# Optimization experiments

Measured on AMD Instinct MI355X. Metric: run time of the kernel, lower is better.

The kernel has to match this reference:

```python
import jax, jax.numpy as jnp
import numpy as np


def setup_inputs() -> dict:
    key = jax.random.key(0)
    ks = jax.random.split(key, 6)
    B, d, S = 256, 512, 196  # batch, hidden dim, spatial locations (14x14)
    return {
        "memory_state": jax.random.normal(ks[0], (B, d), dtype=jnp.float32),
        "ctrl_state": jax.random.normal(ks[1], (B, d), dtype=jnp.float32),
        "kb_proj": jax.random.normal(ks[2], (B, d, S), dtype=jnp.float32),
        "W_concat": jax.random.normal(ks[3], (d, d), dtype=jnp.float32) * (1.0 / np.sqrt(d)),
        "b_concat": jax.random.normal(ks[4], (d,), dtype=jnp.float32) * 0.01,
        "w_attn": jax.random.normal(ks[5], (d,), dtype=jnp.float32) * (1.0 / np.sqrt(d)),
    }


def reference(memory_state, ctrl_state, kb_proj, W_concat, b_concat, w_attn):
    # I_elements: [B, S, d] -- elementwise gating of knowledge base by memory
    I_t = memory_state[:, :, None] * kb_proj           # [B, d, S]
    I_t = jnp.transpose(I_t, (0, 2, 1))                # [B, S, d]
    # concat_layer (torch Linear: x @ W^T + b) + residual with kb_proj
    concat = jnp.einsum('bsd,ed->bse', I_t, W_concat) + b_concat
    concat = concat + jnp.transpose(kb_proj, (0, 2, 1))  # [B, S, d]
    # attention logits: (concat * ctrl) @ w_attn -> [B, S]
    rai = jnp.einsum('bsd,d->bs', concat * ctrl_state[:, None, :], w_attn)
    rvi = jax.nn.softmax(rai, axis=1)                  # [B, S]
    # attention-weighted sum over spatial locations -> [B, d]
    read_vector = jnp.einsum('bs,bds->bd', rvi, kb_proj)
    return read_vector
```

## Files before the change

kernel.cpp:

```cpp
#include <hip/hip_runtime.h>
#include <math.h>

#define B 256
#define D 512
#define S 196
#define NCH 8
#define TC 16
#define NT 13

__global__ __launch_bounds__(256) void k_gemm2(
    const float* __restrict__ ctrl, const float* __restrict__ w_attn,
    const float* __restrict__ W, float* __restrict__ gpart) {
    __shared__ float u_s[64][8];
    const int ce = blockIdx.x >> 6;
    const int dh = (blockIdx.x >> 5) & 1;
    const int b0 = (blockIdx.x & 31) * 8;
    const int t = threadIdx.x;
    const int d = dh * 256 + t;
#pragma unroll
    for (int k = t; k < 512; k += 256) {
        const int j = k & 7, el = k >> 3;
        const int e = ce * 64 + el;
        u_s[el][j] = ctrl[(size_t)(b0 + j) * D + e] * w_attn[e];
    }
    __syncthreads();
    float a[8];
#pragma unroll
    for (int j = 0; j < 8; ++j) a[j] = 0.f;
    for (int e0 = 0; e0 < 64; e0 += 4) {
        float wv[4];
#pragma unroll
        for (int i = 0; i < 4; ++i)
            wv[i] = W[(size_t)(ce * 64 + e0 + i) * D + d];
#pragma unroll
        for (int i = 0; i < 4; ++i) {
            const float4 ua = *(const float4*)&u_s[e0 + i][0];
            const float4 ub = *(const float4*)&u_s[e0 + i][4];
            a[0] += ua.x * wv[i]; a[1] += ua.y * wv[i];
            a[2] += ua.z * wv[i]; a[3] += ua.w * wv[i];
            a[4] += ub.x * wv[i]; a[5] += ub.y * wv[i];
            a[6] += ub.z * wv[i]; a[7] += ub.w * wv[i];
        }
    }
#pragma unroll
    for (int j = 0; j < 8; ++j)
        gpart[((size_t)(b0 + j) * NCH + ce) * D + d] = a[j];
}

__global__ __launch_bounds__(1024, 1) void k_online(
    const float* __restrict__ kb, const float* __restrict__ gpart,
    const float* __restrict__ mem, const float* __restrict__ ctrl,
    const float* __restrict__ w_attn, float* __restrict__ out) {
    __shared__ float tile[2][D][TC + 1];
    __shared__ float pr[TC][65];
    __shared__ float rai_t[TC];
    __shared__ float p_s[D];
    __shared__ float oa[2][D];
    __shared__ float Zs[2];
    const int b = blockIdx.x;
    const int t = threadIdx.x;
    const float* base = kb + (size_t)b * D * S;

    const int ld_d = t >> 2, ld_jq = t & 3;
    const int col_lo = 4 * ld_jq;

    float4 v0 = *(const float4*)(base + (size_t)ld_d * S + col_lo);
    float4 v1 = *(const float4*)(base + (size_t)(ld_d + 256) * S + col_lo);

    if (t < D) {
        float s = 0.f;
#pragma unroll
        for (int ce = 0; ce < NCH; ++ce)
            s += gpart[((size_t)b * NCH + ce) * D + t];
        p_s[t] = mem[(size_t)b * D + t] * s +
                 ctrl[(size_t)b * D + t] * w_attn[t];
    }

    tile[0][ld_d][col_lo + 0] = v0.x; tile[0][ld_d][col_lo + 1] = v0.y;
    tile[0][ld_d][col_lo + 2] = v0.z; tile[0][ld_d][col_lo + 3] = v0.w;
    tile[0][ld_d + 256][col_lo + 0] = v1.x;
    tile[0][ld_d + 256][col_lo + 1] = v1.y;
    tile[0][ld_d + 256][col_lo + 2] = v1.z;
    tile[0][ld_d + 256][col_lo + 3] = v1.w;
    __syncthreads();

    const int col = t & 15, dseg = t >> 4;
    const int wvx = t >> 6, l = t & 63;
    const int dow = t >> 1, sh = t & 1;

    float mrun = -1e30f, Zrun = 0.f, oacc = 0.f;

    for (int j = 0; j < NT; ++j) {
        const int cur = j & 1;
        float4 u0 = {0.f, 0.f, 0.f, 0.f}, u1 = {0.f, 0.f, 0.f, 0.f};
        if (j + 1 < NT) {
            const int c0 = (j + 1) * TC + col_lo;
            if (c0 + 3 < S) {
                u0 = *(const float4*)(base + (size_t)ld_d * S + c0);
                u1 = *(const float4*)(base + (size_t)(ld_d + 256) * S + c0);
            }
        }
        float a = 0.f;
#pragma unroll
        for (int i = 0; i < 8; ++i)
            a += p_s[dseg * 8 + i] * tile[cur][dseg * 8 + i][col];
        pr[col][dseg] = a;
        __syncthreads();
        {
            float vs = pr[wvx][l];
#pragma unroll
            for (int o = 1; o < 64; o <<= 1) vs += __shfl_xor(vs, o, 64);
            if (l == 0)
                rai_t[wvx] = (j * TC + wvx < S) ? vs : -1e30f;
        }
        __syncthreads();
        float mt = rai_t[0];
#pragma unroll
        for (int i = 1; i < TC; ++i) mt = fmaxf(mt, rai_t[i]);
        const float mnew = fmaxf(mrun, mt);
        const float f = __expf(mrun - mnew);
        float wexp[8];
        float zadd = 0.f;
#pragma unroll
        for (int i = 0; i < 8; ++i) {
            wexp[i] = __expf(rai_t[sh * 8 + i] - mnew);
            zadd += wexp[i];
        }
        Zrun = Zrun * f + zadd;
        oacc *= f;
#pragma unroll
        for (int i = 0; i < 8; ++i)
            oacc += wexp[i] * tile[cur][dow][sh * 8 + i];
        mrun = mnew;
        if (j + 1 < NT) {
            const int nb = cur ^ 1;
            tile[nb][ld_d][col_lo + 0] = u0.x;
            tile[nb][ld_d][col_lo + 1] = u0.y;
            tile[nb][ld_d][col_lo + 2] = u0.z;
            tile[nb][ld_d][col_lo + 3] = u0.w;
            tile[nb][ld_d + 256][col_lo + 0] = u1.x;
            tile[nb][ld_d + 256][col_lo + 1] = u1.y;
            tile[nb][ld_d + 256][col_lo + 2] = u1.z;
            tile[nb][ld_d + 256][col_lo + 3] = u1.w;
        }
        __syncthreads();
    }

    oa[sh][dow] = oacc;
    if (t == 0) Zs[0] = Zrun;
    if (t == 1) Zs[1] = Zrun;
    __syncthreads();
    if (t < D)
        out[(size_t)b * D + t] = (oa[0][t] + oa[1][t]) / (Zs[0] + Zs[1]);
}

extern "C" void kernel_launch(void* const* d_in, const int* in_sizes, int n_in,
                              void* d_out, int out_size, void* d_ws, size_t ws_size,
                              hipStream_t stream) {
    const float* mem  = (const float*)d_in[0];
    const float* ctrl = (const float*)d_in[1];
    const float* kb   = (const float*)d_in[2];
    const float* W    = (const float*)d_in[3];
    const float* wat  = (const float*)d_in[5];
    float* out = (float*)d_out;

    float* gpart = (float*)d_ws;

    k_gemm2 <<<512, 256,  0, stream>>>(ctrl, wat, W, gpart);
    k_online<<<B,   1024, 0, stream>>>(kb, gpart, mem, ctrl, wat, out);
}
```

Measured before the change: 178.5 us.

## Keep kb tiles in registers and reduce logits with wave shuffles

The online-softmax kernel no longer stages kb tiles in shared memory. Each thread keeps its two float4 slices in registers, computes partial logits, reduces them with cross-lane shuffles plus one small shared buffer, and accumulates the weighted sum directly from registers. That removes the shared tile traffic and one barrier per tile. The pre-GEMM is also re-tiled into 2048 blocks with 16 e-chunks and float4 W loads, which drops its shared memory and barrier but doubles the partial sums that k_online must read and add.

```diff
diff --git a/kernel.cpp b/kernel.cpp
--- a/kernel.cpp
+++ b/kernel.cpp
@@ -4,68 +4,59 @@
 #define B 256
 #define D 512
 #define S 196
-#define NCH 8
+#define NCH 16
 #define TC 16
 #define NT 13
 
-__global__ __launch_bounds__(256) void k_gemm2(
+__global__ __launch_bounds__(256) void k_gemm(
     const float* __restrict__ ctrl, const float* __restrict__ w_attn,
     const float* __restrict__ W, float* __restrict__ gpart) {
-    __shared__ float u_s[64][8];
-    const int ce = blockIdx.x >> 6;
-    const int dh = (blockIdx.x >> 5) & 1;
-    const int b0 = (blockIdx.x & 31) * 8;
+    const int bid = blockIdx.x;
+    const int ce = bid & 15;
+    const int dq4 = (bid >> 4) & 3;
+    const int b0 = (bid >> 6) * 8;
     const int t = threadIdx.x;
-    const int d = dh * 256 + t;
+    const int j = t >> 5, dqi = t & 31;
+    const int d = dq4 * 128 + dqi * 4;
+    const int e0 = ce * 32;
+    float u[32];
 #pragma unroll
-    for (int k = t; k < 512; k += 256) {
-        const int j = k & 7, el = k >> 3;
-        const int e = ce * 64 + el;
-        u_s[el][j] = ctrl[(size_t)(b0 + j) * D + e] * w_attn[e];
+    for (int k = 0; k < 8; ++k) {
+        const float4 cv =
+            *(const float4*)(ctrl + (size_t)(b0 + j) * D + e0 + 4 * k);
+        const float4 wv = *(const float4*)(w_attn + e0 + 4 * k);
+        u[4 * k + 0] = cv.x * wv.x; u[4 * k + 1] = cv.y * wv.y;
+        u[4 * k + 2] = cv.z * wv.z; u[4 * k + 3] = cv.w * wv.w;
     }
-    __syncthreads();
-    float a[8];
+    float4 a = {0.f, 0.f, 0.f, 0.f};
 #pragma unroll
-    for (int j = 0; j < 8; ++j) a[j] = 0.f;
-    for (int e0 = 0; e0 < 64; e0 += 4) {
-        float wv[4];
-#pragma unroll
-        for (int i = 0; i < 4; ++i)
-            wv[i] = W[(size_t)(ce * 64 + e0 + i) * D + d];
-#pragma unroll
-        for (int i = 0; i < 4; ++i) {
-            const float4 ua = *(const float4*)&u_s[e0 + i][0];
-            const float4 ub = *(const float4*)&u_s[e0 + i][4];
-            a[0] += ua.x * wv[i]; a[1] += ua.y * wv[i];
-            a[2] += ua.z * wv[i]; a[3] += ua.w * wv[i];
-            a[4] += ub.x * wv[i]; a[5] += ub.y * wv[i];
-            a[6] += ub.z * wv[i]; a[7] += ub.w * wv[i];
-        }
+    for (int e = 0; e < 32; ++e) {
+        const float4 w4 = *(const float4*)(W + (size_t)(e0 + e) * D + d);
+        a.x += u[e] * w4.x; a.y += u[e] * w4.y;
+        a.z += u[e] * w4.z; a.w += u[e] * w4.w;
     }
-#pragma unroll
-    for (int j = 0; j < 8; ++j)
-        gpart[((size_t)(b0 + j) * NCH + ce) * D + d] = a[j];
+    *(float4*)&gpart[((size_t)(b0 + j) * NCH + ce) * D + d] = a;
 }
 
 __global__ __launch_bounds__(1024, 1) void k_online(
     const float* __restrict__ kb, const float* __restrict__ gpart,
     const float* __restrict__ mem, const float* __restrict__ ctrl,
     const float* __restrict__ w_attn, float* __restrict__ out) {
-    __shared__ float tile[2][D][TC + 1];
-    __shared__ float pr[TC][65];
-    __shared__ float rai_t[TC];
     __shared__ float p_s[D];
-    __shared__ float oa[2][D];
-    __shared__ float Zs[2];
+    __shared__ float wpr[2][16][20];
     const int b = blockIdx.x;
     const int t = threadIdx.x;
+    const int l = t & 63, wv = t >> 6;
+    const int rl = t >> 2;
+    const int jq = t & 3;
     const float* base = kb + (size_t)b * D * S;
 
-    const int ld_d = t >> 2, ld_jq = t & 3;
-    const int col_lo = 4 * ld_jq;
-
-    float4 v0 = *(const float4*)(base + (size_t)ld_d * S + col_lo);
-    float4 v1 = *(const float4*)(base + (size_t)(ld_d + 256) * S + col_lo);
+    float4 ca, cb, na, nb;
+    {
+        const int c0 = 4 * jq;
+        ca = *(const float4*)(base + (size_t)rl * S + c0);
+        cb = *(const float4*)(base + (size_t)(rl + 256) * S + c0);
+    }
 
     if (t < D) {
         float s = 0.f;
@@ -75,83 +66,78 @@
         p_s[t] = mem[(size_t)b * D + t] * s +
                  ctrl[(size_t)b * D + t] * w_attn[t];
     }
+    __syncthreads();
+    const float p0 = p_s[rl], p1 = p_s[rl + 256];
 
-    tile[0][ld_d][col_lo + 0] = v0.x; tile[0][ld_d][col_lo + 1] = v0.y;
-    tile[0][ld_d][col_lo + 2] = v0.z; tile[0][ld_d][col_lo + 3] = v0.w;
-    tile[0][ld_d + 256][col_lo + 0] = v1.x;
-    tile[0][ld_d + 256][col_lo + 1] = v1.y;
-    tile[0][ld_d + 256][col_lo + 2] = v1.z;
-    tile[0][ld_d + 256][col_lo + 3] = v1.w;
-    __syncthreads();
+    float mrun = -1e30f, Zrun = 0.f, o0 = 0.f, o1 = 0.f;
 
-    const int col = t & 15, dseg = t >> 4;
-    const int wvx = t >> 6, l = t & 63;
-    const int dow = t >> 1, sh = t & 1;
-
-    float mrun = -1e30f, Zrun = 0.f, oacc = 0.f;
-
-    for (int j = 0; j < NT; ++j) {
-        const int cur = j & 1;
-        float4 u0 = {0.f, 0.f, 0.f, 0.f}, u1 = {0.f, 0.f, 0.f, 0.f};
-        if (j + 1 < NT) {
-            const int c0 = (j + 1) * TC + col_lo;
+    for (int jt = 0; jt < NT; ++jt) {
+        const int buf = jt & 1;
+        if (jt + 1 < NT) {
+            const int c0 = (jt + 1) * TC + 4 * jq;
             if (c0 + 3 < S) {
-                u0 = *(const float4*)(base + (size_t)ld_d * S + c0);
-                u1 = *(const float4*)(base + (size_t)(ld_d + 256) * S + c0);
+                na = *(const float4*)(base + (size_t)rl * S + c0);
+                nb = *(const float4*)(base + (size_t)(rl + 256) * S + c0);
+            } else {
+                na = make_float4(0.f, 0.f, 0.f, 0.f);
+                nb = make_float4(0.f, 0.f, 0.f, 0.f);
             }
         }
-        float a = 0.f;
+        float lp[4];
+        lp[0] = p0 * ca.x + p1 * cb.x;
+        lp[1] = p0 * ca.y + p1 * cb.y;
+        lp[2] = p0 * ca.z + p1 * cb.z;
+        lp[3] = p0 * ca.w + p1 * cb.w;
 #pragma unroll
-        for (int i = 0; i < 8; ++i)
-            a += p_s[dseg * 8 + i] * tile[cur][dseg * 8 + i][col];
-        pr[col][dseg] = a;
-        __syncthreads();
-        {
-            float vs = pr[wvx][l];
-#pragma unroll
-            for (int o = 1; o < 64; o <<= 1) vs += __shfl_xor(vs, o, 64);
-            if (l == 0)
-                rai_t[wvx] = (j * TC + wvx < S) ? vs : -1e30f;
+        for (int o = 4; o < 64; o <<= 1) {
+            lp[0] += __shfl_xor(lp[0], o, 64);
+            lp[1] += __shfl_xor(lp[1], o, 64);
+            lp[2] += __shfl_xor(lp[2], o, 64);
+            lp[3] += __shfl_xor(lp[3], o, 64);
+        }
+        if (l < 4) {
+            wpr[buf][4 * l + 0][wv] = lp[0];
+            wpr[buf][4 * l + 1][wv] = lp[1];
+            wpr[buf][4 * l + 2][wv] = lp[2];
+            wpr[buf][4 * l + 3][wv] = lp[3];
         }
         __syncthreads();
-        float mt = rai_t[0];
+        const float4 q0 = *(const float4*)&wpr[buf][l & 15][0];
+        const float4 q1 = *(const float4*)&wpr[buf][l & 15][4];
+        const float4 q2 = *(const float4*)&wpr[buf][l & 15][8];
+        const float4 q3 = *(const float4*)&wpr[buf][l & 15][12];
+        float r = ((q0.x + q0.y) + (q0.z + q0.w)) +
+                  ((q1.x + q1.y) + (q1.z + q1.w)) +
+                  ((q2.x + q2.y) + (q2.z + q2.w)) +
+                  ((q3.x + q3.y) + (q3.z + q3.w));
+        r = (jt * TC + (l & 15) < S) ? r : -1e30f;
+        float mt = r;
 #pragma unroll
-        for (int i = 1; i < TC; ++i) mt = fmaxf(mt, rai_t[i]);
+        for (int o = 1; o < 16; o <<= 1)
+            mt = fmaxf(mt, __shfl_xor(mt, o, 64));
         const float mnew = fmaxf(mrun, mt);
         const float f = __expf(mrun - mnew);
-        float wexp[8];
-        float zadd = 0.f;
-#pragma unroll
-        for (int i = 0; i < 8; ++i) {
-            wexp[i] = __expf(rai_t[sh * 8 + i] - mnew);
-            zadd += wexp[i];
-        }
-        Zrun = Zrun * f + zadd;
-        oacc *= f;
-#pragma unroll
-        for (int i = 0; i < 8; ++i)
-            oacc += wexp[i] * tile[cur][dow][sh * 8 + i];
         mrun = mnew;
-        if (j + 1 < NT) {
-            const int nb = cur ^ 1;
-            tile[nb][ld_d][col_lo + 0] = u0.x;
-            tile[nb][ld_d][col_lo + 1] = u0.y;
-            tile[nb][ld_d][col_lo + 2] = u0.z;
-            tile[nb][ld_d][col_lo + 3] = u0.w;
-            tile[nb][ld_d + 256][col_lo + 0] = u1.x;
-            tile[nb][ld_d + 256][col_lo + 1] = u1.y;
-            tile[nb][ld_d + 256][col_lo + 2] = u1.z;
-            tile[nb][ld_d + 256][col_lo + 3] = u1.w;
-        }
-        __syncthreads();
+        const int sb = l & 48;
+        const float r0 = __shfl(r, sb + 4 * jq + 0, 64);
+        const float r1 = __shfl(r, sb + 4 * jq + 1, 64);
+        const float r2 = __shfl(r, sb + 4 * jq + 2, 64);
+        const float r3 = __shfl(r, sb + 4 * jq + 3, 64);
+        const float w0 = __expf(r0 - mnew), w1 = __expf(r1 - mnew);
+        const float w2 = __expf(r2 - mnew), w3 = __expf(r3 - mnew);
+        Zrun = Zrun * f + ((w0 + w1) + (w2 + w3));
+        o0 = o0 * f + (w0 * ca.x + w1 * ca.y + w2 * ca.z + w3 * ca.w);
+        o1 = o1 * f + (w0 * cb.x + w1 * cb.y + w2 * cb.z + w3 * cb.w);
+        ca = na; cb = nb;
     }
 
-    oa[sh][dow] = oacc;
-    if (t == 0) Zs[0] = Zrun;
-    if (t == 1) Zs[1] = Zrun;
-    __syncthreads();
-    if (t < D)
-        out[(size_t)b * D + t] = (oa[0][t] + oa[1][t]) / (Zs[0] + Zs[1]);
+    o0 += __shfl_xor(o0, 1, 64); o0 += __shfl_xor(o0, 2, 64);
+    o1 += __shfl_xor(o1, 1, 64); o1 += __shfl_xor(o1, 2, 64);
+    Zrun += __shfl_xor(Zrun, 1, 64); Zrun += __shfl_xor(Zrun, 2, 64);
+    if (jq == 0) {
+        out[(size_t)b * D + rl]       = o0 / Zrun;
+        out[(size_t)b * D + rl + 256] = o1 / Zrun;
+    }
 }
 
 extern "C" void kernel_launch(void* const* d_in, const int* in_sizes, int n_in,
@@ -166,6 +152,6 @@
 
     float* gpart = (float*)d_ws;
 
-    k_gemm2 <<<512, 256,  0, stream>>>(ctrl, wat, W, gpart);
-    k_online<<<B,   1024, 0, stream>>>(kb, gpart, mem, ctrl, wat, out);
+    k_gemm  <<<2048, 256,  0, stream>>>(ctrl, wat, W, gpart);
+    k_online<<<B,    1024, 0, stream>>>(kb, gpart, mem, ctrl, wat, out);
 }
```

New measurement: 187.3 us. +4.9%, slower.

## Split softmax-weighted read over spatial halves with a separate merge kernel

Applied to the files above, without the earlier changes.

Each batch row's 196 spatial columns are now split across two 512-thread blocks, doubling the block count. The kb tile is stored transposed in shared memory. The online running-max rescaling is dropped in favour of plain exp of the logits. A small merge kernel then sums the two partial outputs and partial normalisers and divides. This is meant to raise occupancy and shorten the per-block serial loop. In exchange it adds a third launch and workspace traffic, and it risks exp overflow when logits are large.

```diff
diff --git a/kernel.cpp b/kernel.cpp
--- a/kernel.cpp
+++ b/kernel.cpp
@@ -6,7 +6,7 @@
 #define S 196
 #define NCH 8
 #define TC 16
-#define NT 13
+#define RP 521
 
 __global__ __launch_bounds__(256) void k_gemm2(
     const float* __restrict__ ctrl, const float* __restrict__ w_attn,
@@ -47,27 +47,51 @@
         gpart[((size_t)(b0 + j) * NCH + ce) * D + d] = a[j];
 }
 
-__global__ __launch_bounds__(1024, 1) void k_online(
+__global__ __launch_bounds__(512, 4) void k_half(
     const float* __restrict__ kb, const float* __restrict__ gpart,
     const float* __restrict__ mem, const float* __restrict__ ctrl,
-    const float* __restrict__ w_attn, float* __restrict__ out) {
-    __shared__ float tile[2][D][TC + 1];
-    __shared__ float pr[TC][65];
-    __shared__ float rai_t[TC];
+    const float* __restrict__ w_attn, float* __restrict__ opart,
+    float* __restrict__ zpart) {
+    __shared__ float tile[2][TC][RP];
     __shared__ float p_s[D];
-    __shared__ float oa[2][D];
-    __shared__ float Zs[2];
-    const int b = blockIdx.x;
+    __shared__ float pr[TC][33];
+    __shared__ float w_s[TC];
+    const int bid = blockIdx.x;
+    const int b = bid >> 1, h = bid & 1;
     const int t = threadIdx.x;
+    const int c0 = h ? 112 : 0;
+    const int NTb = h ? 6 : 7;
     const float* base = kb + (size_t)b * D * S;
 
-    const int ld_d = t >> 2, ld_jq = t & 3;
-    const int col_lo = 4 * ld_jq;
+    const int q = t & 3, r0 = t >> 2;
 
-    float4 v0 = *(const float4*)(base + (size_t)ld_d * S + col_lo);
-    float4 v1 = *(const float4*)(base + (size_t)(ld_d + 256) * S + col_lo);
+#define STAGE(BUF)                                                        \
+    do {                                                                  \
+        tile[BUF][4 * q + 0][r0] = n0.x; tile[BUF][4 * q + 1][r0] = n0.y; \
+        tile[BUF][4 * q + 2][r0] = n0.z; tile[BUF][4 * q + 3][r0] = n0.w; \
+        tile[BUF][4 * q + 0][r0 + 128] = n1.x;                            \
+        tile[BUF][4 * q + 1][r0 + 128] = n1.y;                            \
+        tile[BUF][4 * q + 2][r0 + 128] = n1.z;                            \
+        tile[BUF][4 * q + 3][r0 + 128] = n1.w;                            \
+        tile[BUF][4 * q + 0][r0 + 256] = n2.x;                            \
+        tile[BUF][4 * q + 1][r0 + 256] = n2.y;                            \
+        tile[BUF][4 * q + 2][r0 + 256] = n2.z;                            \
+        tile[BUF][4 * q + 3][r0 + 256] = n2.w;                            \
+        tile[BUF][4 * q + 0][r0 + 384] = n3.x;                            \
+        tile[BUF][4 * q + 1][r0 + 384] = n3.y;                            \
+        tile[BUF][4 * q + 2][r0 + 384] = n3.z;                            \
+        tile[BUF][4 * q + 3][r0 + 384] = n3.w;                            \
+    } while (0)
 
-    if (t < D) {
+    float4 n0, n1, n2, n3;
+    {
+        const int cq = c0 + 4 * q;
+        n0 = *(const float4*)(base + (size_t)r0 * S + cq);
+        n1 = *(const float4*)(base + (size_t)(r0 + 128) * S + cq);
+        n2 = *(const float4*)(base + (size_t)(r0 + 256) * S + cq);
+        n3 = *(const float4*)(base + (size_t)(r0 + 384) * S + cq);
+    }
+    {
         float s = 0.f;
 #pragma unroll
         for (int ce = 0; ce < NCH; ++ce)
@@ -75,83 +99,75 @@
         p_s[t] = mem[(size_t)b * D + t] * s +
                  ctrl[(size_t)b * D + t] * w_attn[t];
     }
-
-    tile[0][ld_d][col_lo + 0] = v0.x; tile[0][ld_d][col_lo + 1] = v0.y;
-    tile[0][ld_d][col_lo + 2] = v0.z; tile[0][ld_d][col_lo + 3] = v0.w;
-    tile[0][ld_d + 256][col_lo + 0] = v1.x;
-    tile[0][ld_d + 256][col_lo + 1] = v1.y;
-    tile[0][ld_d + 256][col_lo + 2] = v1.z;
-    tile[0][ld_d + 256][col_lo + 3] = v1.w;
+    STAGE(0);
     __syncthreads();
 
-    const int col = t & 15, dseg = t >> 4;
-    const int wvx = t >> 6, l = t & 63;
-    const int dow = t >> 1, sh = t & 1;
+    const int c = t & 15, g = t >> 4;
+    const int l = t & 63, wv = t >> 6;
+    float Zrun = 0.f, oacc = 0.f;
 
-    float mrun = -1e30f, Zrun = 0.f, oacc = 0.f;
-
-    for (int j = 0; j < NT; ++j) {
-        const int cur = j & 1;
-        float4 u0 = {0.f, 0.f, 0.f, 0.f}, u1 = {0.f, 0.f, 0.f, 0.f};
-        if (j + 1 < NT) {
-            const int c0 = (j + 1) * TC + col_lo;
-            if (c0 + 3 < S) {
-                u0 = *(const float4*)(base + (size_t)ld_d * S + c0);
-                u1 = *(const float4*)(base + (size_t)(ld_d + 256) * S + c0);
+    for (int jt = 0; jt < NTb; ++jt) {
+        const int buf = jt & 1;
+        if (jt + 1 < NTb) {
+            const int cq = c0 + (jt + 1) * TC + 4 * q;
+            if (cq + 4 <= S) {
+                n0 = *(const float4*)(base + (size_t)r0 * S + cq);
+                n1 = *(const float4*)(base + (size_t)(r0 + 128) * S + cq);
+                n2 = *(const float4*)(base + (size_t)(r0 + 256) * S + cq);
+                n3 = *(const float4*)(base + (size_t)(r0 + 384) * S + cq);
+            } else {
+                n0 = n1 = n2 = n3 = make_float4(0.f, 0.f, 0.f, 0.f);
             }
         }
         float a = 0.f;
 #pragma unroll
-        for (int i = 0; i < 8; ++i)
-            a += p_s[dseg * 8 + i] * tile[cur][dseg * 8 + i][col];
-        pr[col][dseg] = a;
+        for (int i = 0; i < 16; ++i)
+            a += p_s[16 * g + i] * tile[buf][c][16 * g + i];
+        pr[c][g] = a;
         __syncthreads();
         {
-            float vs = pr[wvx][l];
-#pragma unroll
-            for (int o = 1; o < 64; o <<= 1) vs += __shfl_xor(vs, o, 64);
-            if (l == 0)
-                rai_t[wvx] = (j * TC + wvx < S) ? vs : -1e30f;
+            const int col = wv + 8 * (l >> 5);
+            float v = pr[col][l & 31];
+            v += __shfl_xor(v, 1, 64);  v += __shfl_xor(v, 2, 64);
+            v += __shfl_xor(v, 4, 64);  v += __shfl_xor(v, 8, 64);
+            v += __shfl_xor(v, 16, 64);
+            if ((l & 31) == 0)
+                w_s[col] = (c0 + jt * TC + col < S) ? __expf(v) : 0.f;
         }
+        if (jt + 1 < NTb) STAGE(buf ^ 1);
         __syncthreads();
-        float mt = rai_t[0];
-#pragma unroll
-        for (int i = 1; i < TC; ++i) mt = fmaxf(mt, rai_t[i]);
-        const float mnew = fmaxf(mrun, mt);
-        const float f = __expf(mrun - mnew);
-        float wexp[8];
-        float zadd = 0.f;
-#pragma unroll
-        for (int i = 0; i < 8; ++i) {
-            wexp[i] = __expf(rai_t[sh * 8 + i] - mnew);
-            zadd += wexp[i];
-        }
-        Zrun = Zrun * f + zadd;
-        oacc *= f;
-#pragma unroll
-        for (int i = 0; i < 8; ++i)
-            oacc += wexp[i] * tile[cur][dow][sh * 8 + i];
-        mrun = mnew;
-        if (j + 1 < NT) {
-            const int nb = cur ^ 1;
-            tile[nb][ld_d][col_lo + 0] = u0.x;
-            tile[nb][ld_d][col_lo + 1] = u0.y;
-            tile[nb][ld_d][col_lo + 2] = u0.z;
-            tile[nb][ld_d][col_lo + 3] = u0.w;
-            tile[nb][ld_d + 256][col_lo + 0] = u1.x;
-            tile[nb][ld_d + 256][col_lo + 1] = u1.y;
-            tile[nb][ld_d + 256][col_lo + 2] = u1.z;
-            tile[nb][ld_d + 256][col_lo + 3] = u1.w;
-        }
-        __syncthreads();
+        const float4 wa = *(const float4*)&w_s[0];
+        const float4 wb = *(const float4*)&w_s[4];
+        const float4 wc = *(const float4*)&w_s[8];
+        const float4 wd = *(const float4*)&w_s[12];
+        Zrun += ((wa.x + wa.y) + (wa.z + wa.w)) +
+                ((wb.x + wb.y) + (wb.z + wb.w)) +
+                ((wc.x + wc.y) + (wc.z + wc.w)) +
+                ((wd.x + wd.y) + (wd.z + wd.w));
+        float o = 0.f;
+        o += wa.x * tile[buf][0][t];  o += wa.y * tile[buf][1][t];
+        o += wa.z * tile[buf][2][t];  o += wa.w * tile[buf][3][t];
+        o += wb.x * tile[buf][4][t];  o += wb.y * tile[buf][5][t];
+        o += wb.z * tile[buf][6][t];  o += wb.w * tile[buf][7][t];
+        o += wc.x * tile[buf][8][t];  o += wc.y * tile[buf][9][t];
+        o += wc.z * tile[buf][10][t]; o += wc.w * tile[buf][11][t];
+        o += wd.x * tile[buf][12][t]; o += wd.y * tile[buf][13][t];
+        o += wd.z * tile[buf][14][t]; o += wd.w * tile[buf][15][t];
+        oacc += o;
     }
+#undef STAGE
 
-    oa[sh][dow] = oacc;
-    if (t == 0) Zs[0] = Zrun;
-    if (t == 1) Zs[1] = Zrun;
-    __syncthreads();
-    if (t < D)
-        out[(size_t)b * D + t] = (oa[0][t] + oa[1][t]) / (Zs[0] + Zs[1]);
+    opart[((size_t)h * B + b) * D + t] = oacc;
+    if (t == 0) zpart[h * B + b] = Zrun;
+}
+
+__global__ __launch_bounds__(512) void k_merge(
+    const float* __restrict__ opart, const float* __restrict__ zpart,
+    float* __restrict__ out) {
+    const int b = blockIdx.x, t = threadIdx.x;
+    const float z = zpart[b] + zpart[B + b];
+    out[(size_t)b * D + t] =
+        (opart[(size_t)b * D + t] + opart[((size_t)B + b) * D + t]) / z;
 }
 
 extern "C" void kernel_launch(void* const* d_in, const int* in_sizes, int n_in,
@@ -165,7 +181,10 @@
     float* out = (float*)d_out;
 
     float* gpart = (float*)d_ws;
+    float* opart = gpart + (size_t)B * NCH * D;
+    float* zpart = opart + (size_t)2 * B * D;
 
-    k_gemm2 <<<512, 256,  0, stream>>>(ctrl, wat, W, gpart);
-    k_online<<<B,   1024, 0, stream>>>(kb, gpart, mem, ctrl, wat, out);
+    k_gemm2<<<512,   256, 0, stream>>>(ctrl, wat, W, gpart);
+    k_half <<<2 * B, 512, 0, stream>>>(kb, gpart, mem, ctrl, wat, opart, zpart);
+    k_merge<<<B,     512, 0, stream>>>(opart, zpart, out);
 }
```

New measurement: 183.3 us. 1.03x slower.

## Deepen kb prefetch, vectorize LDS tiles, and drop online-softmax max tracking

Applied to the files above, without the earlier changes.

The attention kernel now prefetches kb two tiles ahead using register pairs, with the loop manually unrolled by two. The shared tiles are padded to a stride of 20 so float4 stores and loads are possible. The logit reduction is regrouped: each thread handles 4 rows by 2 columns, and one wave finishes the sum with float4 LDS reads and shuffles. A custom barrier waits only on LDS counters, so global prefetches can stay in flight across the barrier. The running-max rescaling is removed and exp is applied to raw logits, which saves the per-tile max and rescale work but can overflow if the logits grow large.

```diff
diff --git a/kernel.cpp b/kernel.cpp
--- a/kernel.cpp
+++ b/kernel.cpp
@@ -7,6 +7,11 @@
 #define NCH 8
 #define TC 16
 #define NT 13
+#define PAD 20
+
+#define BAR() do { asm volatile("s_waitcnt lgkmcnt(0)" ::: "memory"); \
+                   __builtin_amdgcn_s_barrier();                      \
+                   asm volatile("" ::: "memory"); } while (0)
 
 __global__ __launch_bounds__(256) void k_gemm2(
     const float* __restrict__ ctrl, const float* __restrict__ w_attn,
@@ -51,9 +56,9 @@
     const float* __restrict__ kb, const float* __restrict__ gpart,
     const float* __restrict__ mem, const float* __restrict__ ctrl,
     const float* __restrict__ w_attn, float* __restrict__ out) {
-    __shared__ float tile[2][D][TC + 1];
-    __shared__ float pr[TC][65];
-    __shared__ float rai_t[TC];
+    __shared__ __align__(16) float tile[2][D][PAD];
+    __shared__ __align__(16) float pr[TC][132];
+    __shared__ __align__(16) float w_s[TC];
     __shared__ float p_s[D];
     __shared__ float oa[2][D];
     __shared__ float Zs[2];
@@ -61,8 +66,7 @@
     const int t = threadIdx.x;
     const float* base = kb + (size_t)b * D * S;
 
-    const int ld_d = t >> 2, ld_jq = t & 3;
-    const int col_lo = 4 * ld_jq;
+    const int ld_d = t >> 2, col_lo = 4 * (t & 3);
 
     float4 v0 = *(const float4*)(base + (size_t)ld_d * S + col_lo);
     float4 v1 = *(const float4*)(base + (size_t)(ld_d + 256) * S + col_lo);
@@ -75,76 +79,81 @@
         p_s[t] = mem[(size_t)b * D + t] * s +
                  ctrl[(size_t)b * D + t] * w_attn[t];
     }
+    *(float4*)&tile[0][ld_d][col_lo] = v0;
+    *(float4*)&tile[0][ld_d + 256][col_lo] = v1;
 
-    tile[0][ld_d][col_lo + 0] = v0.x; tile[0][ld_d][col_lo + 1] = v0.y;
-    tile[0][ld_d][col_lo + 2] = v0.z; tile[0][ld_d][col_lo + 3] = v0.w;
-    tile[0][ld_d + 256][col_lo + 0] = v1.x;
-    tile[0][ld_d + 256][col_lo + 1] = v1.y;
-    tile[0][ld_d + 256][col_lo + 2] = v1.z;
-    tile[0][ld_d + 256][col_lo + 3] = v1.w;
-    __syncthreads();
+    float4 rAa = *(const float4*)(base + (size_t)ld_d * S + TC + col_lo);
+    float4 rAb = *(const float4*)(base + (size_t)(ld_d + 256) * S + TC + col_lo);
+    float4 rBa = *(const float4*)(base + (size_t)ld_d * S + 2 * TC + col_lo);
+    float4 rBb = *(const float4*)(base + (size_t)(ld_d + 256) * S + 2 * TC + col_lo);
 
-    const int col = t & 15, dseg = t >> 4;
-    const int wvx = t >> 6, l = t & 63;
+    BAR();
+
+    const int c2 = t & 7, dg = t >> 3;
+    const float pv0 = p_s[dg * 4 + 0], pv1 = p_s[dg * 4 + 1];
+    const float pv2 = p_s[dg * 4 + 2], pv3 = p_s[dg * 4 + 3];
     const int dow = t >> 1, sh = t & 1;
 
-    float mrun = -1e30f, Zrun = 0.f, oacc = 0.f;
+    float Zrun = 0.f, oacc = 0.f;
 
-    for (int j = 0; j < NT; ++j) {
-        const int cur = j & 1;
-        float4 u0 = {0.f, 0.f, 0.f, 0.f}, u1 = {0.f, 0.f, 0.f, 0.f};
-        if (j + 1 < NT) {
-            const int c0 = (j + 1) * TC + col_lo;
-            if (c0 + 3 < S) {
-                u0 = *(const float4*)(base + (size_t)ld_d * S + c0);
-                u1 = *(const float4*)(base + (size_t)(ld_d + 256) * S + c0);
-            }
-        }
-        float a = 0.f;
-#pragma unroll
-        for (int i = 0; i < 8; ++i)
-            a += p_s[dseg * 8 + i] * tile[cur][dseg * 8 + i][col];
-        pr[col][dseg] = a;
-        __syncthreads();
-        {
-            float vs = pr[wvx][l];
-#pragma unroll
-            for (int o = 1; o < 64; o <<= 1) vs += __shfl_xor(vs, o, 64);
-            if (l == 0)
-                rai_t[wvx] = (j * TC + wvx < S) ? vs : -1e30f;
-        }
-        __syncthreads();
-        float mt = rai_t[0];
-#pragma unroll
-        for (int i = 1; i < TC; ++i) mt = fmaxf(mt, rai_t[i]);
-        const float mnew = fmaxf(mrun, mt);
-        const float f = __expf(mrun - mnew);
-        float wexp[8];
-        float zadd = 0.f;
-#pragma unroll
-        for (int i = 0; i < 8; ++i) {
-            wexp[i] = __expf(rai_t[sh * 8 + i] - mnew);
-            zadd += wexp[i];
-        }
-        Zrun = Zrun * f + zadd;
-        oacc *= f;
-#pragma unroll
-        for (int i = 0; i < 8; ++i)
-            oacc += wexp[i] * tile[cur][dow][sh * 8 + i];
-        mrun = mnew;
-        if (j + 1 < NT) {
-            const int nb = cur ^ 1;
-            tile[nb][ld_d][col_lo + 0] = u0.x;
-            tile[nb][ld_d][col_lo + 1] = u0.y;
-            tile[nb][ld_d][col_lo + 2] = u0.z;
-            tile[nb][ld_d][col_lo + 3] = u0.w;
-            tile[nb][ld_d + 256][col_lo + 0] = u1.x;
-            tile[nb][ld_d + 256][col_lo + 1] = u1.y;
-            tile[nb][ld_d + 256][col_lo + 2] = u1.z;
-            tile[nb][ld_d + 256][col_lo + 3] = u1.w;
-        }
-        __syncthreads();
+#define BODY(J, CUR, Ra, Rb)                                                  \
+    do {                                                                      \
+                                    \
+        const float2 q0 = *(const float2*)&tile[CUR][dg * 4 + 0][2 * c2];     \
+        const float2 q1 = *(const float2*)&tile[CUR][dg * 4 + 1][2 * c2];     \
+        const float2 q2 = *(const float2*)&tile[CUR][dg * 4 + 2][2 * c2];     \
+        const float2 q3 = *(const float2*)&tile[CUR][dg * 4 + 3][2 * c2];     \
+        pr[2 * c2 + 0][dg] =                                                  \
+            pv0 * q0.x + pv1 * q1.x + pv2 * q2.x + pv3 * q3.x;                \
+        pr[2 * c2 + 1][dg] =                                                  \
+            pv0 * q0.y + pv1 * q1.y + pv2 * q2.y + pv3 * q3.y;                \
+        BAR();                                                                \
+                          \
+        if (t < 64) {                                                         \
+            const int c = t >> 2, q = t & 3;                                  \
+            float s = 0.f;                                                    \
+            _Pragma("unroll")                                                 \
+            for (int k = 0; k < 8; ++k) {                                     \
+                const float4 v = *(const float4*)&pr[c][q * 32 + 4 * k];      \
+                s += (v.x + v.y) + (v.z + v.w);                               \
+            }                                                                 \
+            s += __shfl_xor(s, 1, 64);                                        \
+            s += __shfl_xor(s, 2, 64);                                        \
+            if (q == 0) w_s[c] = ((J) * TC + c < S) ? __expf(s) : 0.f;        \
+        }                                                                     \
+        BAR();                                                                \
+                          \
+        const float4 wA = *(const float4*)&w_s[sh * 8];                       \
+        const float4 wB = *(const float4*)&w_s[sh * 8 + 4];                   \
+        Zrun += ((wA.x + wA.y) + (wA.z + wA.w)) +                             \
+                ((wB.x + wB.y) + (wB.z + wB.w));                              \
+        const float4 ta = *(const float4*)&tile[CUR][dow][sh * 8];            \
+        const float4 tb = *(const float4*)&tile[CUR][dow][sh * 8 + 4];        \
+        oacc += wA.x * ta.x + wA.y * ta.y + wA.z * ta.z + wA.w * ta.w +       \
+                wB.x * tb.x + wB.y * tb.y + wB.z * tb.z + wB.w * tb.w;        \
+                      \
+        if ((J) + 1 < NT) {                                                   \
+            *(float4*)&tile[(CUR) ^ 1][ld_d][col_lo] = Ra;                    \
+            *(float4*)&tile[(CUR) ^ 1][ld_d + 256][col_lo] = Rb;              \
+        }                                                                     \
+        if ((J) + 3 < NT) {                                                   \
+            const int cq = ((J) + 3) * TC + col_lo;                           \
+            if (cq + 3 < S) {                                                 \
+                Ra = *(const float4*)(base + (size_t)ld_d * S + cq);          \
+                Rb = *(const float4*)(base + (size_t)(ld_d + 256) * S + cq);  \
+            } else {                                                          \
+                Ra = make_float4(0.f, 0.f, 0.f, 0.f);                         \
+                Rb = make_float4(0.f, 0.f, 0.f, 0.f);                         \
+            }                                                                 \
+        }                                                                     \
+        BAR();                                                                \
+    } while (0)
+
+    for (int j = 0; j < NT; j += 2) {
+        BODY(j, 0, rAa, rAb);
+        if (j + 1 < NT) BODY(j + 1, 1, rBa, rBb);
     }
+#undef BODY
 
     oa[sh][dow] = oacc;
     if (t == 0) Zs[0] = Zrun;
```

New measurement: 175.4 us. Within noise of the previous version (-1.7%).
